# Kernel optimization log

Measured on AMD Instinct MI355X. Metric: run time of the kernel, lower is better.

The kernel has to match this reference:

```python
import jax, jax.numpy as jnp
import numpy as np

N = 100_000      # nodes
E = 1_600_000    # edges (avg degree 16)
D_IN = 64        # input feature size
H = 4            # num_heads
F = 16           # out_feats per head
EFST = 1e-3      # norm clamp from source


def setup_inputs() -> dict:
    key = jax.random.key(0)
    k0, k1, k2, k3, k4, k5 = jax.random.split(key, 6)
    feat = jax.random.normal(k0, (N, D_IN), dtype=jnp.float32)
    src = jax.random.randint(k1, (E,), 0, N, dtype=jnp.int32)
    dst = jax.random.randint(k2, (E,), 0, N, dtype=jnp.int32)
    W = jax.random.normal(k3, (H * F, D_IN), dtype=jnp.float32) * 0.1   # fc.weight
    attn_l = jax.random.normal(k4, (H, F), dtype=jnp.float32) * 0.1
    attn_r = jax.random.normal(k5, (H, F), dtype=jnp.float32) * 0.1
    return dict(feat=feat, src=src, dst=dst, W=W, attn_l=attn_l, attn_r=attn_r)


def reference(feat, src, dst, W, attn_l, attn_r):
    n = feat.shape[0]
    h, f = attn_l.shape
    # fc projection -> (N, H, F)
    z = (feat @ W.T).reshape(n, h, f)
    # attention logits per node per head
    el = jnp.einsum('nhf,hf->nh', z, attn_l)  # (N, H)
    er = jnp.einsum('nhf,hf->nh', z, attn_r)  # (N, H)
    # per-node squared-feature sums over heads, clamped (source: ft[ft<efst]=efst)
    s = jnp.maximum(jnp.sum(z * z, axis=1), EFST)  # (N, F)
    inv_s = 1.0 / s
    # edge-level gathers
    zu = z[src]                                   # (E, H, F)
    zv = z[dst]                                   # (E, H, F)
    edp = jnp.einsum('ehf,ehf->eh', zu, zv)       # u_dot_v(ft, ftd)
    edp_ftfd = jnp.einsum('ef,ef->e', inv_s[src], inv_s[dst])  # per-edge scalar
    e_sum = el[src] + er[dst]                     # u_add_v(el, er) -> (E, H)
    escore = jax.nn.relu(edp * edp_ftfd[:, None]) * e_sum       # (E, H)
    # edge_softmax over incoming edges per dst node, per head
    m = jax.ops.segment_max(escore, dst, num_segments=n)        # (N, H)
    m = jnp.where(jnp.isfinite(m), m, 0.0)                      # empty segments
    ex = jnp.exp(escore - m[dst])                               # (E, H)
    denom = jax.ops.segment_sum(ex, dst, num_segments=n)        # (N, H)
    a = ex / jnp.where(denom[dst] > 0, denom[dst], 1.0)         # (E, H)
    # aggregate: u_mul_e(ft, a) then sum per dst
    out = jax.ops.segment_sum(a[:, :, None] * zu, dst, num_segments=n)  # (N, H, F)
    return out
```

## Files before the change

kernel.cpp:

```cpp
#include <hip/hip_runtime.h>
#include <hip/hip_fp16.h>
#include <math.h>

#define DIN 64
#define LOG2E 1.44269504f
#define DEFER_THR 11.5415603f
#define BKT_CAP 5120
#define EPB 2048
#define SRC_MASK 0x1FFFFF


__device__ __forceinline__ float fast_exp2(float x) {
    float r; asm("v_exp_f32 %0, %1" : "=v"(r) : "v"(x)); return r;
}
__device__ __forceinline__ int rfl(int x) { return __builtin_amdgcn_readfirstlane(x); }

typedef _Float16 half2_t __attribute__((ext_vector_type(2)));
typedef _Float16 f16x8 __attribute__((ext_vector_type(8)));
typedef float f32x4 __attribute__((ext_vector_type(4)));

__device__ __forceinline__ float fdot2(float a_raw, float b_raw, float acc) {
    half2_t a = __builtin_bit_cast(half2_t, a_raw);
    half2_t b = __builtin_bit_cast(half2_t, b_raw);
    return __builtin_amdgcn_fdot2(a, b, acc, false);
}

__device__ __forceinline__ void split8(const float* p, f16x8& hi, f16x8& lo) {
    float4 v0 = *(const float4*)p;
    float4 v1 = *(const float4*)(p + 4);
    float vv[8] = {v0.x, v0.y, v0.z, v0.w, v1.x, v1.y, v1.z, v1.w};
#pragma unroll
    for (int i = 0; i < 8; i++) {
        _Float16 h = (_Float16)vv[i];
        hi[i] = h;
        lo[i] = (_Float16)(vv[i] - (float)h);
    }
}

template<int CTRL>
__device__ __forceinline__ float dppmov(float x) {
    union { float f; int i; } u, r;
    u.f = x;
    r.i = __builtin_amdgcn_update_dpp(0, u.i, CTRL, 0xF, 0xF, true);
    return r.f;
}
__device__ __forceinline__ float rowsum16(float x) {
    x += dppmov<0xB1>(x);
    x += dppmov<0x4E>(x);
    x += dppmov<0x124>(x);
    x += dppmov<0x128>(x);
    return x;
}
__device__ __forceinline__ float rowsum8(float x) {
    x += dppmov<0xB1>(x);
    x += dppmov<0x4E>(x);
    x += dppmov<0x141>(x);
    return x;
}

__global__ __launch_bounds__(256) void build_all(
    const float* __restrict__ feat, const float* __restrict__ W,
    const float* __restrict__ attn_l, const float* __restrict__ attn_r,
    const int* __restrict__ src, const int* __restrict__ dst, int e_n,
    int* __restrict__ gcur, unsigned int* __restrict__ pairs,
    __half* __restrict__ zrec, float* __restrict__ misc, int n, int nbkt)
{
    int bid = blockIdx.x;
    int r = bid % 3;
    if (r < 2) {
        int base = ((bid / 3) * 2 + r) * EPB;
        int tid = threadIdx.x;
        int wv = tid >> 6;
        __shared__ int hist4[4][400];
        __shared__ int curb[400];
        for (int i = tid; i < 4 * 400; i += 256) ((int*)hist4)[i] = 0;
        __syncthreads();
        int d[8], s[8];
#pragma unroll
        for (int k = 0; k < 8; k++) {
            int idx = base + k * 256 + tid;
            bool val = idx < e_n;
            d[k] = val ? dst[idx] : -1;
            s[k] = val ? src[idx] : 0;
            if (val) atomicAdd(&hist4[wv][d[k] >> 8], 1);
        }
        __syncthreads();
        for (int i = tid; i < nbkt; i += 256) {
            int c = hist4[0][i] + hist4[1][i] + hist4[2][i] + hist4[3][i];
            curb[i] = (c > 0) ? atomicAdd(&gcur[i], c) : 0;
        }
        __syncthreads();
#pragma unroll
        for (int k = 0; k < 8; k++) {
            if (d[k] >= 0) {
                int b = d[k] >> 8;
                int pos = atomicAdd(&curb[b], 1);
                if (pos < BKT_CAP)
                    pairs[(size_t)b * BKT_CAP + pos] =
                        (unsigned int)s[k] | ((unsigned int)(d[k] & 255) << 21);
            }
        }
        return;
    }
    int mb = bid / 3;

    int lane = threadIdx.x & 63;
    int col = lane & 15;
    int kg  = lane >> 4;

    f16x8 bhi[4][2], blo[4][2];
#pragma unroll
    for (int t = 0; t < 4; t++) {
#pragma unroll
        for (int kh = 0; kh < 2; kh++) {
            const float* wp = W + (size_t)(16 * t + col) * 64 + kh * 32 + kg * 8;
            split8(wp, bhi[t][kh], blo[t][kh]);
        }
    }

    float al[4], ar[4];
#pragma unroll
    for (int t = 0; t < 4; t++) {
        al[t] = attn_l[t * 16 + col];
        ar[t] = attn_r[t * 16 + col];
    }

    int wti = mb * 4 + (threadIdx.x >> 6);

#pragma unroll 1
    for (int it = 0; it < 4; it++) {
        int nb = (wti * 4 + it) * 16;
        if (nb >= n) break;
        int arow = nb + col; if (arow > n - 1) arow = n - 1;
        const float* ap = feat + (size_t)arow * 64 + kg * 8;
        f16x8 ahi0, alo0, ahi1, alo1;
        split8(ap, ahi0, alo0);
        split8(ap + 32, ahi1, alo1);

        f32x4 c[4];
#pragma unroll
        for (int t = 0; t < 4; t++) {
            f32x4 acc = {0.f, 0.f, 0.f, 0.f};
            acc = __builtin_amdgcn_mfma_f32_16x16x32_f16(alo0, bhi[t][0], acc, 0, 0, 0);
            acc = __builtin_amdgcn_mfma_f32_16x16x32_f16(ahi0, blo[t][0], acc, 0, 0, 0);
            acc = __builtin_amdgcn_mfma_f32_16x16x32_f16(ahi0, bhi[t][0], acc, 0, 0, 0);
            acc = __builtin_amdgcn_mfma_f32_16x16x32_f16(alo1, bhi[t][1], acc, 0, 0, 0);
            acc = __builtin_amdgcn_mfma_f32_16x16x32_f16(ahi1, blo[t][1], acc, 0, 0, 0);
            acc = __builtin_amdgcn_mfma_f32_16x16x32_f16(ahi1, bhi[t][1], acc, 0, 0, 0);
            c[t] = acc;
        }

#pragma unroll
        for (int j = 0; j < 4; j++) {
            int rr = nb + kg * 4 + j;
            if (rr >= n) continue;
            float z0 = c[0][j], z1 = c[1][j], z2 = c[2][j], z3 = c[3][j];

            float sq = z0 * z0 + z1 * z1 + z2 * z2 + z3 * z3;
            float isv = 1.0f / fmaxf(sq, 1e-3f);

            float e0 = rowsum16(z0 * al[0]) * LOG2E;
            float e1 = rowsum16(z1 * al[1]) * LOG2E;
            float e2 = rowsum16(z2 * al[2]) * LOG2E;
            float e3 = rowsum16(z3 * al[3]) * LOG2E;
            float r0 = rowsum16(z0 * ar[0]) * LOG2E;
            float r1 = rowsum16(z1 * ar[1]) * LOG2E;
            float r2 = rowsum16(z2 * ar[2]) * LOG2E;
            float r3 = rowsum16(z3 * ar[3]) * LOG2E;

            __half* zp = zrec + (size_t)rr * 64;
            zp[col]      = __float2half_rn(z0);
            zp[16 + col] = __float2half_rn(z1);
            zp[32 + col] = __float2half_rn(z2);
            zp[48 + col] = __float2half_rn(z3);

            float* mf = misc + (size_t)rr * 16;
            ((__half*)mf)[col] = __float2half_rn(isv);
            if (col == 0) {
                mf[8]  = e0; mf[9]  = e1; mf[10] = e2; mf[11] = e3;
                mf[12] = r0; mf[13] = r1; mf[14] = r2; mf[15] = r3;
            }
        }
    }
}

__global__ __launch_bounds__(256) void bucket_csr(
    const unsigned int* __restrict__ pairs, const int* __restrict__ gcur,
    int* __restrict__ perm, int2* __restrict__ srow, int n)
{
    int b = blockIdx.x;
    int tid = threadIdx.x;
    int count = min(gcur[b], BKT_CAP);

    __shared__ unsigned int plds[BKT_CAP];
    __shared__ int hist[256], sums[256], cur2[256];

    for (int i = tid; i < count; i += 256) plds[i] = pairs[(size_t)b * BKT_CAP + i];
    hist[tid] = 0;
    __syncthreads();
    for (int i = tid; i < count; i += 256) atomicAdd(&hist[plds[i] >> 21], 1);
    __syncthreads();
    int hv = hist[tid];
    sums[tid] = hv;
    __syncthreads();
    for (int off = 1; off < 256; off <<= 1) {
        int x = (tid >= off) ? sums[tid - off] : 0;
        __syncthreads();
        sums[tid] += x;
        __syncthreads();
    }
    int excl = sums[tid] - hv;
    int v = b * 256 + tid;
    if (v < n) srow[v] = make_int2(b * BKT_CAP + excl, hv);
    cur2[tid] = excl;
    __syncthreads();
    for (int i = tid; i < count; i += 256) {
        unsigned int p = plds[i];
        int pos = atomicAdd(&cur2[p >> 21], 1);
        perm[(size_t)b * BKT_CAP + pos] = (int)(p & SRC_MASK);
    }
}

__global__ __launch_bounds__(256) void node_fused(
    const __half* __restrict__ zrec, const float* __restrict__ misc,
    const int* __restrict__ perm, const int2* __restrict__ srow,
    float* __restrict__ out, int n)
{
    int lane = threadIdx.x & 63;
    int slot = lane >> 3;
    int l8   = lane & 7;
    int h    = l8 >> 1;
    int v = blockIdx.x * 4 + (threadIdx.x >> 6);
    if (v >= n) return;
    v = rfl(v);

    int2 sr = srow[v];
    int start = rfl(sr.x), len = rfl(sr.y);

    float* op = out + (size_t)v * 64 + 8 * l8;
    if (len == 0) {
        if (slot == 0) {
            *(float4*)op = make_float4(0.f, 0.f, 0.f, 0.f);
            *(float4*)(op + 4) = make_float4(0.f, 0.f, 0.f, 0.f);
        }
        return;
    }

    float4 zvr = *(const float4*)(zrec + (size_t)v * 64 + 8 * l8);
    const float* mv = misc + (size_t)v * 16;
    float ivr = mv[l8];
    float erv = mv[12 + h];

    int idx = start + slot;
    float w = (slot < len) ? 1.f : 0.f;
    int u = (slot < len) ? perm[idx] : v;

    float m = -INFINITY, denom = 0.f;
    float4 accA = make_float4(0.f, 0.f, 0.f, 0.f);
    float4 accB = make_float4(0.f, 0.f, 0.f, 0.f);
    int lmax = (len + 7) >> 3;

    for (int it = 0; it < lmax; ++it) {
        int rn = len - (8 * (it + 1) + slot);
        int un = (rn > 0) ? perm[idx + 8] : v;
        float wn = (rn > 0) ? 1.f : 0.f;

        float4 zur = *(const float4*)(zrec + (size_t)u * 64 + 8 * l8);
        const float* mu = misc + (size_t)u * 16;
        float iur = mu[l8];
        float eu = mu[8 + h];

        float edp = fdot2(zur.x, zvr.x,
                    fdot2(zur.y, zvr.y,
                    fdot2(zur.z, zvr.z,
                    fdot2(zur.w, zvr.w, 0.f))));
        edp += dppmov<0xB1>(edp);
        float ffp = rowsum8(fdot2(iur, ivr, 0.f));
        float s = fmaxf(edp * ffp, 0.f) * (eu + erv) * w;

        if (s > m + DEFER_THR) {
            float c = fast_exp2(m - s);
            denom *= c;
            accA.x *= c; accA.y *= c; accA.z *= c; accA.w *= c;
            accB.x *= c; accB.y *= c; accB.z *= c; accB.w *= c;
            m = s;
        }
        float p = fast_exp2(s - m) * w;
        denom += p;
        float2 z0 = __half22float2(*(__half2*)&zur.x);
        float2 z1 = __half22float2(*(__half2*)&zur.y);
        float2 z2 = __half22float2(*(__half2*)&zur.z);
        float2 z3 = __half22float2(*(__half2*)&zur.w);
        accA.x = fmaf(p, z0.x, accA.x); accA.y = fmaf(p, z0.y, accA.y);
        accA.z = fmaf(p, z1.x, accA.z); accA.w = fmaf(p, z1.y, accA.w);
        accB.x = fmaf(p, z2.x, accB.x); accB.y = fmaf(p, z2.y, accB.y);
        accB.z = fmaf(p, z3.x, accB.z); accB.w = fmaf(p, z3.y, accB.w);

        u = un; w = wn; idx += 8;
    }

    {
        float om = dppmov<0x128>(m);
        float od = dppmov<0x128>(denom);
        float oA0 = dppmov<0x128>(accA.x), oA1 = dppmov<0x128>(accA.y);
        float oA2 = dppmov<0x128>(accA.z), oA3 = dppmov<0x128>(accA.w);
        float oB0 = dppmov<0x128>(accB.x), oB1 = dppmov<0x128>(accB.y);
        float oB2 = dppmov<0x128>(accB.z), oB3 = dppmov<0x128>(accB.w);
        float mm = fmaxf(m, om);
        float cs = fast_exp2(m - mm), co = fast_exp2(om - mm);
        denom = denom * cs + od * co;
        accA.x = accA.x * cs + oA0 * co; accA.y = accA.y * cs + oA1 * co;
        accA.z = accA.z * cs + oA2 * co; accA.w = accA.w * cs + oA3 * co;
        accB.x = accB.x * cs + oB0 * co; accB.y = accB.y * cs + oB1 * co;
        accB.z = accB.z * cs + oB2 * co; accB.w = accB.w * cs + oB3 * co;
        m = mm;
    }
#pragma unroll
    for (int off = 16; off <= 32; off <<= 1) {
        float om = __shfl_xor(m, off);
        float od = __shfl_xor(denom, off);
        float oA0 = __shfl_xor(accA.x, off), oA1 = __shfl_xor(accA.y, off);
        float oA2 = __shfl_xor(accA.z, off), oA3 = __shfl_xor(accA.w, off);
        float oB0 = __shfl_xor(accB.x, off), oB1 = __shfl_xor(accB.y, off);
        float oB2 = __shfl_xor(accB.z, off), oB3 = __shfl_xor(accB.w, off);
        float mm = fmaxf(m, om);
        float cs = fast_exp2(m - mm), co = fast_exp2(om - mm);
        denom = denom * cs + od * co;
        accA.x = accA.x * cs + oA0 * co; accA.y = accA.y * cs + oA1 * co;
        accA.z = accA.z * cs + oA2 * co; accA.w = accA.w * cs + oA3 * co;
        accB.x = accB.x * cs + oB0 * co; accB.y = accB.y * cs + oB1 * co;
        accB.z = accB.z * cs + oB2 * co; accB.w = accB.w * cs + oB3 * co;
        m = mm;
    }

    if (slot == 0) {
        float inv = 1.0f / denom;
        *(float4*)op = make_float4(accA.x * inv, accA.y * inv, accA.z * inv, accA.w * inv);
        *(float4*)(op + 4) = make_float4(accB.x * inv, accB.y * inv, accB.z * inv, accB.w * inv);
    }
}

extern "C" void kernel_launch(void* const* d_in, const int* in_sizes, int n_in,
                              void* d_out, int out_size, void* d_ws, size_t ws_size,
                              hipStream_t stream)
{
    const float* feat   = (const float*)d_in[0];
    const int*   src    = (const int*)d_in[1];
    const int*   dst    = (const int*)d_in[2];
    const float* W      = (const float*)d_in[3];
    const float* attn_l = (const float*)d_in[4];
    const float* attn_r = (const float*)d_in[5];
    float* out = (float*)d_out;

    const int n   = in_sizes[0] / DIN;
    const int e_n = in_sizes[1];
    const int nbkt = (n + 255) / 256;

    __half*       zrec  = (__half*)d_ws;
    float*        misc  = (float*)(zrec + (size_t)n * 64);
    unsigned int* pairs = (unsigned int*)(misc + (size_t)n * 16);
    int*          perm  = (int*)(pairs + (size_t)nbkt * BKT_CAP);
    int2*         srow  = (int2*)(perm + (size_t)nbkt * BKT_CAP);
    int*          gcur  = (int*)(srow + n);

    hipMemsetAsync(gcur, 0, (size_t)nbkt * sizeof(int), stream);

    hipLaunchKernelGGL(build_all, dim3(nbkt * 3), dim3(256), 0, stream,
                       feat, W, attn_l, attn_r, src, dst, e_n, gcur, pairs, zrec, misc, n, nbkt);

    hipLaunchKernelGGL(bucket_csr, dim3(nbkt), dim3(256), 0, stream,
                       pairs, gcur, perm, srow, n);

    hipLaunchKernelGGL(node_fused, dim3((n + 3) / 4), dim3(256), 0, stream,
                       zrec, misc, perm, srow, out, n);
}
```

Measured before the change: 117.0 us.

## Fuse bucket CSR build with node aggregation using shared-memory permutation

```diff
diff --git a/kernel.cpp b/kernel.cpp
--- a/kernel.cpp
+++ b/kernel.cpp
@@ -5,10 +5,9 @@
 #define DIN 64
 #define LOG2E 1.44269504f
 #define DEFER_THR 11.5415603f
-#define BKT_CAP 5120
+#define BKT_CAP 2560
 #define EPB 2048
 #define SRC_MASK 0x1FFFFF
-
 
 __device__ __forceinline__ float fast_exp2(float x) {
     float r; asm("v_exp_f32 %0, %1" : "=v"(r) : "v"(x)); return r;
@@ -71,9 +70,9 @@
         int base = ((bid / 3) * 2 + r) * EPB;
         int tid = threadIdx.x;
         int wv = tid >> 6;
-        __shared__ int hist4[4][400];
-        __shared__ int curb[400];
-        for (int i = tid; i < 4 * 400; i += 256) ((int*)hist4)[i] = 0;
+        __shared__ int hist4[4][800];
+        __shared__ int curb[800];
+        for (int i = tid; i < 4 * 800; i += 256) ((int*)hist4)[i] = 0;
         __syncthreads();
         int d[8], s[8];
 #pragma unroll
@@ -82,7 +81,7 @@
             bool val = idx < e_n;
             d[k] = val ? dst[idx] : -1;
             s[k] = val ? src[idx] : 0;
-            if (val) atomicAdd(&hist4[wv][d[k] >> 8], 1);
+            if (val) atomicAdd(&hist4[wv][d[k] >> 7], 1);
         }
         __syncthreads();
         for (int i = tid; i < nbkt; i += 256) {
@@ -93,11 +92,11 @@
 #pragma unroll
         for (int k = 0; k < 8; k++) {
             if (d[k] >= 0) {
-                int b = d[k] >> 8;
+                int b = d[k] >> 7;
                 int pos = atomicAdd(&curb[b], 1);
                 if (pos < BKT_CAP)
                     pairs[(size_t)b * BKT_CAP + pos] =
-                        (unsigned int)s[k] | ((unsigned int)(d[k] & 255) << 21);
+                        (unsigned int)s[k] | ((unsigned int)(d[k] & 127) << 21);
             }
         }
         return;
@@ -184,159 +183,153 @@
     }
 }
 
-__global__ __launch_bounds__(256) void bucket_csr(
+__global__ __launch_bounds__(256) void sort_aggregate(
     const unsigned int* __restrict__ pairs, const int* __restrict__ gcur,
-    int* __restrict__ perm, int2* __restrict__ srow, int n)
+    const __half* __restrict__ zrec, const float* __restrict__ misc,
+    float* __restrict__ out, int n)
 {
     int b = blockIdx.x;
     int tid = threadIdx.x;
     int count = min(gcur[b], BKT_CAP);
 
     __shared__ unsigned int plds[BKT_CAP];
-    __shared__ int hist[256], sums[256], cur2[256];
+    __shared__ unsigned int sperm[BKT_CAP + 8];
+    __shared__ int hist[128], sums[128], cur2[128], sstart[128];
 
     for (int i = tid; i < count; i += 256) plds[i] = pairs[(size_t)b * BKT_CAP + i];
-    hist[tid] = 0;
+    if (tid < 128) hist[tid] = 0;
     __syncthreads();
     for (int i = tid; i < count; i += 256) atomicAdd(&hist[plds[i] >> 21], 1);
     __syncthreads();
-    int hv = hist[tid];
-    sums[tid] = hv;
-    __syncthreads();
-    for (int off = 1; off < 256; off <<= 1) {
-        int x = (tid >= off) ? sums[tid - off] : 0;
-        __syncthreads();
-        sums[tid] += x;
-        __syncthreads();
-    }
-    int excl = sums[tid] - hv;
-    int v = b * 256 + tid;
-    if (v < n) srow[v] = make_int2(b * BKT_CAP + excl, hv);
-    cur2[tid] = excl;
+    int hv = 0;
+    if (tid < 128) { hv = hist[tid]; sums[tid] = hv; }
+    __syncthreads();
+    for (int off = 1; off < 128; off <<= 1) {
+        int x = (tid < 128 && tid >= off) ? sums[tid - off] : 0;
+        __syncthreads();
+        if (tid < 128) sums[tid] += x;
+        __syncthreads();
+    }
+    if (tid < 128) { sstart[tid] = sums[tid] - hv; cur2[tid] = sums[tid] - hv; }
     __syncthreads();
     for (int i = tid; i < count; i += 256) {
         unsigned int p = plds[i];
         int pos = atomicAdd(&cur2[p >> 21], 1);
-        perm[(size_t)b * BKT_CAP + pos] = (int)(p & SRC_MASK);
-    }
-}
-
-__global__ __launch_bounds__(256) void node_fused(
-    const __half* __restrict__ zrec, const float* __restrict__ misc,
-    const int* __restrict__ perm, const int2* __restrict__ srow,
-    float* __restrict__ out, int n)
-{
-    int lane = threadIdx.x & 63;
+        sperm[pos] = p & SRC_MASK;
+    }
+    __syncthreads();
+
+    int lane = tid & 63;
     int slot = lane >> 3;
     int l8   = lane & 7;
     int h    = l8 >> 1;
-    int v = blockIdx.x * 4 + (threadIdx.x >> 6);
-    if (v >= n) return;
-    v = rfl(v);
-
-    int2 sr = srow[v];
-    int start = rfl(sr.x), len = rfl(sr.y);
-
-    float* op = out + (size_t)v * 64 + 8 * l8;
-    if (len == 0) {
+    int wv   = tid >> 6;
+
+    for (int k = 0; k < 32; ++k) {
+        int dloc = wv * 32 + k;
+        int v = b * 128 + dloc;
+        if (v >= n) break;
+        int start = sstart[dloc];
+        int len   = hist[dloc];
+
+        float* op = out + (size_t)v * 64 + 8 * l8;
+        if (len == 0) {
+            if (slot == 0) {
+                *(float4*)op = make_float4(0.f, 0.f, 0.f, 0.f);
+                *(float4*)(op + 4) = make_float4(0.f, 0.f, 0.f, 0.f);
+            }
+            continue;
+        }
+
+        float4 zvr = *(const float4*)(zrec + (size_t)v * 64 + 8 * l8);
+        const float* mv = misc + (size_t)v * 16;
+        float ivr = mv[l8];
+        float erv = mv[12 + h];
+
+        int idx = start + slot;
+        float m = -INFINITY, denom = 0.f;
+        float4 accA = make_float4(0.f, 0.f, 0.f, 0.f);
+        float4 accB = make_float4(0.f, 0.f, 0.f, 0.f);
+        int lmax = (len + 7) >> 3;
+
+        for (int it = 0; it < lmax; ++it) {
+            int off_e = 8 * it + slot;
+            float w = (off_e < len) ? 1.f : 0.f;
+            int u = (off_e < len) ? (int)sperm[idx] : v;
+
+            float4 zur = *(const float4*)(zrec + (size_t)u * 64 + 8 * l8);
+            const float* mu = misc + (size_t)u * 16;
+            float iur = mu[l8];
+            float eu = mu[8 + h];
+
+            float edp = fdot2(zur.x, zvr.x,
+                        fdot2(zur.y, zvr.y,
+                        fdot2(zur.z, zvr.z,
+                        fdot2(zur.w, zvr.w, 0.f))));
+            edp += dppmov<0xB1>(edp);
+            float ffp = rowsum8(fdot2(iur, ivr, 0.f));
+            float s = fmaxf(edp * ffp, 0.f) * (eu + erv) * w;
+
+            if (s > m + DEFER_THR) {
+                float c = fast_exp2(m - s);
+                denom *= c;
+                accA.x *= c; accA.y *= c; accA.z *= c; accA.w *= c;
+                accB.x *= c; accB.y *= c; accB.z *= c; accB.w *= c;
+                m = s;
+            }
+            float p = fast_exp2(s - m) * w;
+            denom += p;
+            float2 z0 = __half22float2(*(__half2*)&zur.x);
+            float2 z1 = __half22float2(*(__half2*)&zur.y);
+            float2 z2 = __half22float2(*(__half2*)&zur.z);
+            float2 z3 = __half22float2(*(__half2*)&zur.w);
+            accA.x = fmaf(p, z0.x, accA.x); accA.y = fmaf(p, z0.y, accA.y);
+            accA.z = fmaf(p, z1.x, accA.z); accA.w = fmaf(p, z1.y, accA.w);
+            accB.x = fmaf(p, z2.x, accB.x); accB.y = fmaf(p, z2.y, accB.y);
+            accB.z = fmaf(p, z3.x, accB.z); accB.w = fmaf(p, z3.y, accB.w);
+
+            idx += 8;
+        }
+
+        {
+            float om = dppmov<0x128>(m);
+            float od = dppmov<0x128>(denom);
+            float oA0 = dppmov<0x128>(accA.x), oA1 = dppmov<0x128>(accA.y);
+            float oA2 = dppmov<0x128>(accA.z), oA3 = dppmov<0x128>(accA.w);
+            float oB0 = dppmov<0x128>(accB.x), oB1 = dppmov<0x128>(accB.y);
+            float oB2 = dppmov<0x128>(accB.z), oB3 = dppmov<0x128>(accB.w);
+            float mm = fmaxf(m, om);
+            float cs = fast_exp2(m - mm), co = fast_exp2(om - mm);
+            denom = denom * cs + od * co;
+            accA.x = accA.x * cs + oA0 * co; accA.y = accA.y * cs + oA1 * co;
+            accA.z = accA.z * cs + oA2 * co; accA.w = accA.w * cs + oA3 * co;
+            accB.x = accB.x * cs + oB0 * co; accB.y = accB.y * cs + oB1 * co;
+            accB.z = accB.z * cs + oB2 * co; accB.w = accB.w * cs + oB3 * co;
+            m = mm;
+        }
+#pragma unroll
+        for (int off = 16; off <= 32; off <<= 1) {
+            float om = __shfl_xor(m, off);
+            float od = __shfl_xor(denom, off);
+            float oA0 = __shfl_xor(accA.x, off), oA1 = __shfl_xor(accA.y, off);
+            float oA2 = __shfl_xor(accA.z, off), oA3 = __shfl_xor(accA.w, off);
+            float oB0 = __shfl_xor(accB.x, off), oB1 = __shfl_xor(accB.y, off);
+            float oB2 = __shfl_xor(accB.z, off), oB3 = __shfl_xor(accB.w, off);
+            float mm = fmaxf(m, om);
+            float cs = fast_exp2(m - mm), co = fast_exp2(om - mm);
+            denom = denom * cs + od * co;
+            accA.x = accA.x * cs + oA0 * co; accA.y = accA.y * cs + oA1 * co;
+            accA.z = accA.z * cs + oA2 * co; accA.w = accA.w * cs + oA3 * co;
+            accB.x = accB.x * cs + oB0 * co; accB.y = accB.y * cs + oB1 * co;
+            accB.z = accB.z * cs + oB2 * co; accB.w = accB.w * cs + oB3 * co;
+            m = mm;
+        }
+
         if (slot == 0) {
-            *(float4*)op = make_float4(0.f, 0.f, 0.f, 0.f);
-            *(float4*)(op + 4) = make_float4(0.f, 0.f, 0.f, 0.f);
-        }
-        return;
-    }
-
-    float4 zvr = *(const float4*)(zrec + (size_t)v * 64 + 8 * l8);
-    const float* mv = misc + (size_t)v * 16;
-    float ivr = mv[l8];
-    float erv = mv[12 + h];
-
-    int idx = start + slot;
-    float w = (slot < len) ? 1.f : 0.f;
-    int u = (slot < len) ? perm[idx] : v;
-
-    float m = -INFINITY, denom = 0.f;
-    float4 accA = make_float4(0.f, 0.f, 0.f, 0.f);
-    float4 accB = make_float4(0.f, 0.f, 0.f, 0.f);
-    int lmax = (len + 7) >> 3;
-
-    for (int it = 0; it < lmax; ++it) {
-        int rn = len - (8 * (it + 1) + slot);
-        int un = (rn > 0) ? perm[idx + 8] : v;
-        float wn = (rn > 0) ? 1.f : 0.f;
-
-        float4 zur = *(const float4*)(zrec + (size_t)u * 64 + 8 * l8);
-        const float* mu = misc + (size_t)u * 16;
-        float iur = mu[l8];
-        float eu = mu[8 + h];
-
-        float edp = fdot2(zur.x, zvr.x,
-                    fdot2(zur.y, zvr.y,
-                    fdot2(zur.z, zvr.z,
-                    fdot2(zur.w, zvr.w, 0.f))));
-        edp += dppmov<0xB1>(edp);
-        float ffp = rowsum8(fdot2(iur, ivr, 0.f));
-        float s = fmaxf(edp * ffp, 0.f) * (eu + erv) * w;
-
-        if (s > m + DEFER_THR) {
-            float c = fast_exp2(m - s);
-            denom *= c;
-            accA.x *= c; accA.y *= c; accA.z *= c; accA.w *= c;
-            accB.x *= c; accB.y *= c; accB.z *= c; accB.w *= c;
-            m = s;
-        }
-        float p = fast_exp2(s - m) * w;
-        denom += p;
-        float2 z0 = __half22float2(*(__half2*)&zur.x);
-        float2 z1 = __half22float2(*(__half2*)&zur.y);
-        float2 z2 = __half22float2(*(__half2*)&zur.z);
-        float2 z3 = __half22float2(*(__half2*)&zur.w);
-        accA.x = fmaf(p, z0.x, accA.x); accA.y = fmaf(p, z0.y, accA.y);
-        accA.z = fmaf(p, z1.x, accA.z); accA.w = fmaf(p, z1.y, accA.w);
-        accB.x = fmaf(p, z2.x, accB.x); accB.y = fmaf(p, z2.y, accB.y);
-        accB.z = fmaf(p, z3.x, accB.z); accB.w = fmaf(p, z3.y, accB.w);
-
-        u = un; w = wn; idx += 8;
-    }
-
-    {
-        float om = dppmov<0x128>(m);
-        float od = dppmov<0x128>(denom);
-        float oA0 = dppmov<0x128>(accA.x), oA1 = dppmov<0x128>(accA.y);
-        float oA2 = dppmov<0x128>(accA.z), oA3 = dppmov<0x128>(accA.w);
-        float oB0 = dppmov<0x128>(accB.x), oB1 = dppmov<0x128>(accB.y);
-        float oB2 = dppmov<0x128>(accB.z), oB3 = dppmov<0x128>(accB.w);
-        float mm = fmaxf(m, om);
-        float cs = fast_exp2(m - mm), co = fast_exp2(om - mm);
-        denom = denom * cs + od * co;
-        accA.x = accA.x * cs + oA0 * co; accA.y = accA.y * cs + oA1 * co;
-        accA.z = accA.z * cs + oA2 * co; accA.w = accA.w * cs + oA3 * co;
-        accB.x = accB.x * cs + oB0 * co; accB.y = accB.y * cs + oB1 * co;
-        accB.z = accB.z * cs + oB2 * co; accB.w = accB.w * cs + oB3 * co;
-        m = mm;
-    }
-#pragma unroll
-    for (int off = 16; off <= 32; off <<= 1) {
-        float om = __shfl_xor(m, off);
-        float od = __shfl_xor(denom, off);
-        float oA0 = __shfl_xor(accA.x, off), oA1 = __shfl_xor(accA.y, off);
-        float oA2 = __shfl_xor(accA.z, off), oA3 = __shfl_xor(accA.w, off);
-        float oB0 = __shfl_xor(accB.x, off), oB1 = __shfl_xor(accB.y, off);
-        float oB2 = __shfl_xor(accB.z, off), oB3 = __shfl_xor(accB.w, off);
-        float mm = fmaxf(m, om);
-        float cs = fast_exp2(m - mm), co = fast_exp2(om - mm);
-        denom = denom * cs + od * co;
-        accA.x = accA.x * cs + oA0 * co; accA.y = accA.y * cs + oA1 * co;
-        accA.z = accA.z * cs + oA2 * co; accA.w = accA.w * cs + oA3 * co;
-        accB.x = accB.x * cs + oB0 * co; accB.y = accB.y * cs + oB1 * co;
-        accB.z = accB.z * cs + oB2 * co; accB.w = accB.w * cs + oB3 * co;
-        m = mm;
-    }
-
-    if (slot == 0) {
-        float inv = 1.0f / denom;
-        *(float4*)op = make_float4(accA.x * inv, accA.y * inv, accA.z * inv, accA.w * inv);
-        *(float4*)(op + 4) = make_float4(accB.x * inv, accB.y * inv, accB.z * inv, accB.w * inv);
+            float inv = 1.0f / denom;
+            *(float4*)op = make_float4(accA.x * inv, accA.y * inv, accA.z * inv, accA.w * inv);
+            *(float4*)(op + 4) = make_float4(accB.x * inv, accB.y * inv, accB.z * inv, accB.w * inv);
+        }
     }
 }
 
@@ -354,23 +347,19 @@
 
     const int n   = in_sizes[0] / DIN;
     const int e_n = in_sizes[1];
-    const int nbkt = (n + 255) / 256;
+    const int nbkt = (n + 127) / 128;
 
     __half*       zrec  = (__half*)d_ws;
     float*        misc  = (float*)(zrec + (size_t)n * 64);
     unsigned int* pairs = (unsigned int*)(misc + (size_t)n * 16);
-    int*          perm  = (int*)(pairs + (size_t)nbkt * BKT_CAP);
-    int2*         srow  = (int2*)(perm + (size_t)nbkt * BKT_CAP);
-    int*          gcur  = (int*)(srow + n);
+    int*          gcur  = (int*)(pairs + (size_t)nbkt * BKT_CAP);
 
     hipMemsetAsync(gcur, 0, (size_t)nbkt * sizeof(int), stream);
 
-    hipLaunchKernelGGL(build_all, dim3(nbkt * 3), dim3(256), 0, stream,
+    int mmb = (n + 255) / 256;
+    hipLaunchKernelGGL(build_all, dim3(mmb * 3), dim3(256), 0, stream,
                        feat, W, attn_l, attn_r, src, dst, e_n, gcur, pairs, zrec, misc, n, nbkt);
 
-    hipLaunchKernelGGL(bucket_csr, dim3(nbkt), dim3(256), 0, stream,
-                       pairs, gcur, perm, srow, n);
-
-    hipLaunchKernelGGL(node_fused, dim3((n + 3) / 4), dim3(256), 0, stream,
-                       zrec, misc, perm, srow, out, n);
-}
+    hipLaunchKernelGGL(sort_aggregate, dim3(nbkt), dim3(256), 0, stream,
+                       pairs, gcur, zrec, misc, out, n);
+}
```

Result: slower. 138.3 us (+18.3%).
